# Performance work log

Measured on AMD Instinct MI355X. Metric: run time of the kernel, lower is better.

Reference implementation:

```python
import jax, jax.numpy as jnp
import numpy as np

# Dimensions (match init_kwargs / input_specs)
B, T, H, S, R, E = 4, 2048, 1024, 512, 16, 4
F = 6 + 2 * R           # engine_state_feature_dim
ETA = 0.1               # impression_rate
ACC_DECAY = 0.99        # accumulator EMA decay
EPS = 1e-6


def setup_inputs() -> dict:
    key = jax.random.key(0)
    ks = jax.random.split(key, 20)
    n = jax.random.normal
    x = n(ks[0], (B, T, H), jnp.float32)
    # ComplexLinear signal_proj: hidden -> state
    sig_Wr = n(ks[1], (H, S), jnp.float32) / np.sqrt(H).astype(np.float32)
    sig_Wi = n(ks[2], (H, S), jnp.float32) / np.sqrt(H).astype(np.float32)
    sig_br = jnp.zeros((S,), jnp.float32)
    sig_bi = jnp.zeros((S,), jnp.float32)
    # Per-engine complex state projection [E, S, R] and diagonal complex decay [E, R]
    A_r = n(ks[3], (E, S, R), jnp.float32) / np.sqrt(S).astype(np.float32)
    A_i = n(ks[4], (E, S, R), jnp.float32) / np.sqrt(S).astype(np.float32)
    mag = 0.90 + 0.09 * jax.random.uniform(ks[5], (E, R), jnp.float32)
    ph = (2.0 * np.pi) * jax.random.uniform(ks[6], (E, R), jnp.float32)
    lam_r = mag * jnp.cos(ph)
    lam_i = mag * jnp.sin(ph)
    # Per-engine ComplexLinear: feature(F) -> hidden(H)
    eh_Wr = n(ks[7], (E, F, H), jnp.float32) / np.sqrt(F).astype(np.float32)
    eh_Wi = n(ks[8], (E, F, H), jnp.float32) / np.sqrt(F).astype(np.float32)
    eh_br = jnp.zeros((E, H), jnp.float32)
    eh_bi = jnp.zeros((E, H), jnp.float32)
    # Engine fusion ComplexLinear: E*H -> H
    fu_Wr = n(ks[9], (E * H, H), jnp.float32) / np.sqrt(E * H).astype(np.float32)
    fu_Wi = n(ks[10], (E * H, H), jnp.float32) / np.sqrt(E * H).astype(np.float32)
    fu_br = jnp.zeros((H,), jnp.float32)
    fu_bi = jnp.zeros((H,), jnp.float32)
    # Gate: Linear(4H -> H)
    g_W = n(ks[11], (4 * H, H), jnp.float32) / np.sqrt(4 * H).astype(np.float32)
    g_b = jnp.zeros((H,), jnp.float32)
    return dict(x=x, sig_Wr=sig_Wr, sig_Wi=sig_Wi, sig_br=sig_br, sig_bi=sig_bi,
                A_r=A_r, A_i=A_i, lam_r=lam_r, lam_i=lam_i,
                eh_Wr=eh_Wr, eh_Wi=eh_Wi, eh_br=eh_br, eh_bi=eh_bi,
                fu_Wr=fu_Wr, fu_Wi=fu_Wi, fu_br=fu_br, fu_bi=fu_bi,
                g_W=g_W, g_b=g_b)


def _run_engines(ur, ui, lam_r, lam_i):
    """Complex diagonal recurrence over time for all engines jointly.
    ur, ui: [E,B,T,R] complex drive. Returns per-step features [E,B,T,F] (real, imag)."""
    lr = lam_r[:, None, :]  # [E,1,R]
    li = lam_i[:, None, :]

    def step(carry, u):
        hr, hi, acc = carry                      # [E,B,R], [E,B,R], [E,B]
        ur_t, ui_t = u                           # [E,B,R]
        nhr = (1.0 - ETA) * (lr * hr - li * hi) + ETA * ur_t
        nhi = (1.0 - ETA) * (lr * hi + li * hr) + ETA * ui_t
        mag2 = nhr * nhr + nhi * nhi             # [E,B,R]
        m_mean = jnp.mean(mag2, axis=-1)         # [E,B]
        nacc = ACC_DECAY * acc + (1.0 - ACC_DECAY) * m_mean
        inv = jax.lax.rsqrt(m_mean + EPS)[..., None]
        hnr, hni = nhr * inv, nhi * inv          # rms-normalized complex state
        z = jnp.zeros_like(m_mean)
        scal_r = jnp.stack([hnr.mean(-1), hni.mean(-1),
                            jnp.sqrt(m_mean + EPS),
                            jnp.sqrt(jnp.max(mag2, axis=-1) + EPS),
                            nacc, jnp.log1p(nacc)], axis=-1)   # [E,B,6]
        scal_i = jnp.stack([hni.mean(-1), -hnr.mean(-1), z, z, z, z], axis=-1)
        fr = jnp.concatenate([scal_r, hnr, hni], axis=-1)      # [E,B,F]
        fi = jnp.concatenate([scal_i, hni, -hnr], axis=-1)
        return (nhr, nhi, nacc), (fr, fi)

    init = (jnp.zeros((E, B, R), ur.dtype), jnp.zeros((E, B, R), ur.dtype),
            jnp.zeros((E, B), ur.dtype))
    u_seq = (jnp.moveaxis(ur, 2, 0), jnp.moveaxis(ui, 2, 0))   # [T,E,B,R]
    _, (frs, fis) = jax.lax.scan(step, init, u_seq)
    return jnp.moveaxis(frs, 0, 2), jnp.moveaxis(fis, 0, 2)    # [E,B,T,F]


def reference(x, sig_Wr, sig_Wi, sig_br, sig_bi, A_r, A_i, lam_r, lam_i,
              eh_Wr, eh_Wi, eh_br, eh_bi, fu_Wr, fu_Wi, fu_br, fu_bi, g_W, g_b):
    # Complex signal projection of real input: z = (Wr + i Wi)^T x + b
    zr = x @ sig_Wr + sig_br                     # [B,T,S]
    zi = x @ sig_Wi + sig_bi
    # Complex per-engine drive u = A^H-style complex matmul: [E,B,T,R]
    ur = jnp.einsum('bts,esr->ebtr', zr, A_r) - jnp.einsum('bts,esr->ebtr', zi, A_i)
    ui = jnp.einsum('bts,esr->ebtr', zr, A_i) + jnp.einsum('bts,esr->ebtr', zi, A_r)
    fr, fi = _run_engines(ur, ui, lam_r, lam_i)  # [E,B,T,F]
    # Per-engine ComplexLinear feature -> hidden
    yr = (jnp.einsum('ebtf,efh->ebth', fr, eh_Wr)
          - jnp.einsum('ebtf,efh->ebth', fi, eh_Wi)) + eh_br[:, None, None, :]
    yi = (jnp.einsum('ebtf,efh->ebth', fr, eh_Wi)
          + jnp.einsum('ebtf,efh->ebth', fi, eh_Wr)) + eh_bi[:, None, None, :]
    # Concat engines along feature axis -> [B,T,E*H]
    yr_c = jnp.moveaxis(yr, 0, 2).reshape(B, T, E * H)
    yi_c = jnp.moveaxis(yi, 0, 2).reshape(B, T, E * H)
    # Engine fusion ComplexLinear
    frf = yr_c @ fu_Wr - yi_c @ fu_Wi + fu_br    # [B,T,H]
    fif = yr_c @ fu_Wi + yi_c @ fu_Wr + fu_bi
    mag = jnp.sqrt(frf * frf + fif * fif + EPS)
    g = jax.nn.sigmoid(jnp.concatenate([x, frf, fif, mag], axis=-1) @ g_W + g_b)
    return g * frf + (1.0 - g) * x
```

## Files before the change

### kernel.cpp

```cpp
#include <hip/hip_runtime.h>
#include <stdint.h>

#define B_ 4
#define T_ 2048
#define H_ 1024
#define S_ 512
#define R_ 16
#define E_ 4
#define F_ 38
#define BT_ (B_*T_)
#define KF_ 320

typedef __attribute__((ext_vector_type(8))) __bf16 bf16x8;
typedef __attribute__((ext_vector_type(4))) float f32x4;

static __device__ __forceinline__ unsigned short f2bf(float f) {
    unsigned int u = __float_as_uint(f);
    unsigned int r = (u + 0x7fffu + ((u >> 16) & 1u)) >> 16;
    return (unsigned short)r;
}

static __device__ __forceinline__ void gload_lds16(const unsigned short* g, unsigned short* l) {
    __builtin_amdgcn_global_load_lds(
        (const __attribute__((address_space(1))) unsigned int*)g,
        (__attribute__((address_space(3))) unsigned int*)l, 16, 0, 0);
}

template<int EPI>
__global__ __launch_bounds__(256) void k_gemm(
    const unsigned short* __restrict__ A, int lda,
    const unsigned short* __restrict__ BT, int ldb,
    float* __restrict__ C, int ldc,
    const float* __restrict__ bias, int K,
    size_t sA, size_t sB, size_t sC, int nbx,
    const float* __restrict__ aux1, const float* __restrict__ aux2,
    unsigned short* __restrict__ auxO)
{
    A  += (size_t)blockIdx.z * sA;
    BT += (size_t)blockIdx.z * sB;
    C  += (size_t)blockIdx.z * sC;

    int bx, by;
    {
        const int f = blockIdx.x;
        const int nwg = gridDim.x;
        int s;
        if ((nwg & 7) == 0) {
            const int q = nwg >> 3;
            s = (f & 7) * q + (f >> 3);
        } else s = f;
        by = s / nbx; bx = s - by * nbx;
    }

    __shared__ unsigned short As[128 * 32];
    __shared__ unsigned short Bs[128 * 32];
    const int tid = threadIdx.x;
    const int l = tid & 63;
    const int wv = tid >> 6;
    const int wm = wv >> 1, wn = wv & 1;
    const int m16 = l & 15, kg = l >> 4;
    const size_t bm = (size_t)by * 128;
    const size_t bn = (size_t)bx * 128;

    const int slab0 = wv * 2, slab1 = wv * 2 + 1;
    const int rIn = l >> 2;
    const int kOff = (l & 3) * 8;
    const unsigned short* gA0 = A + (bm + slab0 * 16 + rIn) * (size_t)lda + kOff;
    const unsigned short* gA1 = A + (bm + slab1 * 16 + rIn) * (size_t)lda + kOff;
    const unsigned short* gB0 = BT + (bn + slab0 * 16 + rIn) * (size_t)ldb + kOff;
    const unsigned short* gB1 = BT + (bn + slab1 * 16 + rIn) * (size_t)ldb + kOff;
    unsigned short* lA0 = As + slab0 * 512;
    unsigned short* lA1 = As + slab1 * 512;
    unsigned short* lB0 = Bs + slab0 * 512;
    unsigned short* lB1 = Bs + slab1 * 512;

    f32x4 acc[4][4];
#pragma unroll
    for (int i = 0; i < 4; ++i)
#pragma unroll
        for (int j = 0; j < 4; ++j) acc[i][j] = (f32x4){0.f, 0.f, 0.f, 0.f};

    const int nkt = K >> 5;
    for (int kt = 0; kt < nkt; ++kt) {
        gload_lds16(gA0, lA0);
        gload_lds16(gA1, lA1);
        gload_lds16(gB0, lB0);
        gload_lds16(gB1, lB1);
        gA0 += 32; gA1 += 32; gB0 += 32; gB1 += 32;
        __syncthreads();
        bf16x8 af[4], bfr[4];
#pragma unroll
        for (int i = 0; i < 4; ++i)
            af[i] = *(const bf16x8*)&As[(wm * 64 + i * 16 + m16) * 32 + kg * 8];
#pragma unroll
        for (int j = 0; j < 4; ++j)
            bfr[j] = *(const bf16x8*)&Bs[(wn * 64 + j * 16 + m16) * 32 + kg * 8];
#pragma unroll
        for (int i = 0; i < 4; ++i)
#pragma unroll
            for (int j = 0; j < 4; ++j)
                acc[i][j] = __builtin_amdgcn_mfma_f32_16x16x32_bf16(af[i], bfr[j], acc[i][j], 0, 0, 0);
        __syncthreads();
    }

#pragma unroll
    for (int j = 0; j < 4; ++j) {
        const size_t col = bn + wn * 64 + j * 16 + m16;
        const float bv = (EPI == 1) ? 0.f : (bias ? bias[col] : 0.f);
#pragma unroll
        for (int i = 0; i < 4; ++i) {
            const size_t row0 = bm + wm * 64 + i * 16 + kg * 4;
#pragma unroll
            for (int p = 0; p < 4; ++p) {
                const size_t row = row0 + p;
                if constexpr (EPI == 0) {
                    C[row * (size_t)ldc + col] = acc[i][j][p] + bv;
                } else if constexpr (EPI == 1) {
                    atomicAdd(&C[row * (size_t)ldc + col], acc[i][j][p]);
                } else if constexpr (EPI == 2) {
                    const float v = acc[i][j][p] + bv;
                    const float w = __shfl_xor(v, 1, 64);
                    const int h = (int)(col >> 1);
                    if ((col & 1) == 0) {
                        C[row * 1024 + h] = v;
                        auxO[row * 4096 + 1024 + h] = f2bf(v);
                    } else {
                        auxO[row * 4096 + 2048 + h] = f2bf(v);
                        auxO[row * 4096 + 3072 + h] = f2bf(sqrtf(w * w + v * v + 1e-6f));
                    }
                } else {
                    const float z = acc[i][j][p] + bv;
                    const float g = 1.f / (1.f + __expf(-z));
                    const float fr = aux1[row * 1024 + col];
                    const float xv = aux2[row * 1024 + col];
                    C[row * 1024 + col] = fmaf(g, fr - xv, xv);
                }
            }
        }
    }
}

__global__ __launch_bounds__(256) void k_cast_x(const float* __restrict__ x,
                                                unsigned short* __restrict__ Abig)
{
    const int gid = blockIdx.x * 256 + threadIdx.x;
    const int row = gid >> 8;
    const int c4 = (gid & 255) << 2;
    float4 v = *(const float4*)&x[(size_t)row * H_ + c4];
    ushort4 o;
    o.x = f2bf(v.x); o.y = f2bf(v.y); o.z = f2bf(v.z); o.w = f2bf(v.w);
    *(ushort4*)&Abig[(size_t)row * 4096 + c4] = o;
}

__global__ __launch_bounds__(256) void k_gwt(const float* __restrict__ gW,
                                             unsigned short* __restrict__ gWT)
{
    __shared__ float tile[32][33];
    const int tx = threadIdx.x & 31, ty = threadIdx.x >> 5;
    const int k0 = blockIdx.x * 32, n0 = blockIdx.y * 32;
#pragma unroll
    for (int q = 0; q < 4; ++q) {
        int kk = ty * 4 + q;
        tile[kk][tx] = gW[(size_t)(k0 + kk) * H_ + n0 + tx];
    }
    __syncthreads();
#pragma unroll
    for (int q = 0; q < 4; ++q) {
        int nn = ty * 4 + q;
        gWT[(size_t)(n0 + nn) * 4096 + k0 + tx] = f2bf(tile[tx][nn]);
    }
}

__global__ __launch_bounds__(64) void k_wu(const float* __restrict__ sigWr,
                                           const float* __restrict__ sigWi,
                                           const float* __restrict__ A_r,
                                           const float* __restrict__ A_i,
                                           unsigned short* __restrict__ WuT)
{
    __shared__ float swr[S_], swi[S_];
    const int h = blockIdx.x;
    const int tid = threadIdx.x;
    for (int s = tid; s < S_; s += 64) {
        swr[s] = sigWr[(size_t)h * S_ + s];
        swi[s] = sigWi[(size_t)h * S_ + s];
    }
    __syncthreads();
    const int e = tid >> 4, r = tid & 15;
    float a0 = 0.f, a1 = 0.f;
    for (int s = 0; s < S_; ++s) {
        float ar = A_r[((size_t)(e * S_ + s)) * R_ + r];
        float ai = A_i[((size_t)(e * S_ + s)) * R_ + r];
        float wr = swr[s], wi = swi[s];
        a0 += wr * ar - wi * ai;
        a1 += wr * ai + wi * ar;
    }
    WuT[(size_t)tid * H_ + h] = f2bf(a0);
    WuT[(size_t)(64 + tid) * H_ + h] = f2bf(a1);
}

__global__ __launch_bounds__(64) void k_bu(const float* __restrict__ sigbr,
                                           const float* __restrict__ sigbi,
                                           const float* __restrict__ A_r,
                                           const float* __restrict__ A_i,
                                           float* __restrict__ b_u)
{
    const int n = blockIdx.x;
    const int lane = threadIdx.x;
    const int m = n & 63;
    const int e = m >> 4, r = m & 15;
    const bool hi = n >= 64;
    float acc = 0.f;
    for (int s = lane; s < S_; s += 64) {
        float ar = A_r[((size_t)(e * S_ + s)) * R_ + r];
        float ai = A_i[((size_t)(e * S_ + s)) * R_ + r];
        float br = sigbr[s], bi = sigbi[s];
        acc += hi ? (br * ai + bi * ar) : (br * ar - bi * ai);
    }
#pragma unroll
    for (int st = 32; st; st >>= 1) acc += __shfl_down(acc, st, 64);
    if (lane == 0) b_u[n] = acc;
}

__global__ __launch_bounds__(256) void k_uinit(const float* __restrict__ b_u,
                                               float* __restrict__ U)
{
    const int gid = blockIdx.x * 256 + threadIdx.x;
    U[gid] = b_u[gid & 127];
}

__global__ __launch_bounds__(256) void k_prepA(const float* __restrict__ ehWr,
                                               const float* __restrict__ ehWi,
                                               const float* __restrict__ ehbr,
                                               const float* __restrict__ ehbi,
                                               unsigned short* __restrict__ Ac)
{
    const int gid = blockIdx.x * 256 + threadIdx.x;
    const int e = gid >> 16;
    const int rem = gid & 65535;
    const int row = rem >> 9;
    const int k = (rem & 511) << 2;
    float4 f = {0.f, 0.f, 0.f, 0.f};
    if (row < F_) {
        const float* src = (k < 1024) ? ehWr + ((size_t)(e * F_ + row)) * 1024 + k
                                      : ehWi + ((size_t)(e * F_ + row)) * 1024 + (k - 1024);
        f = *(const float4*)src;
    } else if (row == F_) {
        const float* src = (k < 1024) ? ehbr + (size_t)e * 1024 + k
                                      : ehbi + (size_t)e * 1024 + (k - 1024);
        f = *(const float4*)src;
    }
    ushort4 o;
    o.x = f2bf(f.x); o.y = f2bf(f.y); o.z = f2bf(f.z); o.w = f2bf(f.w);
    *(ushort4*)&Ac[(size_t)gid * 4] = o;
}

__global__ __launch_bounds__(256) void k_prepB(const float* __restrict__ fuWr,
                                               const float* __restrict__ fuWi,
                                               unsigned short* __restrict__ Bc)
{
    __shared__ float tR[32][33], tI[32][33];
    const int e = blockIdx.z;
    const int k0 = blockIdx.x * 32;
    const int h0 = blockIdx.y * 32;
    const int tx = threadIdx.x & 31, ty = threadIdx.x >> 5;
    const float* fr = fuWr + ((size_t)e * 1024 + k0) * 1024 + h0;
    const float* fi = fuWi + ((size_t)e * 1024 + k0) * 1024 + h0;
#pragma unroll
    for (int q = 0; q < 4; ++q) {
        int kk = ty * 4 + q;
        tR[kk][tx] = fr[(size_t)kk * 1024 + tx];
        tI[kk][tx] = fi[(size_t)kk * 1024 + tx];
    }
    __syncthreads();
    unsigned short* Be = Bc + (size_t)e * 2048 * 2048;
#pragma unroll
    for (int q = 0; q < 4; ++q) {
        int rr = ty * 4 + q;
        float vR = tR[tx][rr], vI = tI[tx][rr];
        size_t rowLo = (size_t)(h0 + rr) * 2048;
        size_t rowHi = (size_t)(1024 + h0 + rr) * 2048;
        Be[rowLo + k0 + tx]        = f2bf(vR);
        Be[rowLo + 1024 + k0 + tx] = f2bf(-vI);
        Be[rowHi + k0 + tx]        = f2bf(vI);
        Be[rowHi + 1024 + k0 + tx] = f2bf(vR);
    }
}

__global__ __launch_bounds__(256) void k_w2t(const float* __restrict__ C,
                                             unsigned short* __restrict__ W2T)
{
    const int gid = blockIdx.x * 256 + threadIdx.x;
    const int n = gid / KF_;
    const int k = gid - n * KF_;
    const int h = n >> 1;
    const int s = n & 1;
    float v = 0.f;
    if (k < 304) {
        const int fp = (k < 152) ? k : k - 152;
        const int e = fp / F_;
        const int f = fp - e * F_;
        const float* Ce = C + ((size_t)e * 128 + f) * 2048;
        const float mr = Ce[h], mi = Ce[1024 + h];
        if (s == 0) v = (k < 152) ? mr : -mi;
        else        v = (k < 152) ? mi :  mr;
    }
    W2T[gid] = f2bf(v);
}

__global__ __launch_bounds__(256) void k_b2(const float* __restrict__ fubr,
                                            const float* __restrict__ fubi,
                                            const float* __restrict__ C,
                                            float* __restrict__ b2)
{
    const int n = blockIdx.x * 256 + threadIdx.x;
    const int h = n >> 1;
    const int s = n & 1;
    const int colOld = s * 1024 + h;
    float v = s ? fubi[h] : fubr[h];
#pragma unroll
    for (int e = 0; e < 4; ++e)
        v += C[(size_t)e * 128 * 2048 + (size_t)F_ * 2048 + colOld];
    b2[n] = v;
}

__global__ __launch_bounds__(64) void k_scan(const float* __restrict__ U,
                                             const float* __restrict__ lam_r,
                                             const float* __restrict__ lam_i,
                                             float* __restrict__ Hr, float* __restrict__ Hi)
{
    const int wid = blockIdx.x;
    const int b = wid >> 6, ch = wid & 63;
    const int lane = threadIdx.x;
    const float cr = 0.9f * lam_r[ch];
    const float ci = 0.9f * lam_i[ch];
    const float* Ub = U + (size_t)b * T_ * 128;
    const int t0 = lane * 32;
    float ur[32], ui[32];
#pragma unroll
    for (int j = 0; j < 32; ++j) {
        ur[j] = Ub[(size_t)(t0 + j) * 128 + ch];
        ui[j] = Ub[(size_t)(t0 + j) * 128 + 64 + ch];
    }
    float hr = 0.f, hi = 0.f;
#pragma unroll
    for (int j = 0; j < 32; ++j) {
        float nr = fmaf(cr, hr, fmaf(-ci, hi, 0.1f * ur[j]));
        float ni = fmaf(cr, hi, fmaf(ci, hr, 0.1f * ui[j]));
        hr = nr; hi = ni;
    }
    float dr = cr, di = ci;
#pragma unroll
    for (int q = 0; q < 5; ++q) { float t = dr*dr - di*di; di = 2.f*dr*di; dr = t; }
    float xr = hr, xi = hi;
#pragma unroll
    for (int st = 1; st < 64; st <<= 1) {
        float yr = __shfl_up(xr, (unsigned)st, 64);
        float yi = __shfl_up(xi, (unsigned)st, 64);
        if (lane >= st) {
            float nxr = fmaf(dr, yr, fmaf(-di, yi, xr));
            float nxi = fmaf(dr, yi, fmaf(di, yr, xi));
            xr = nxr; xi = nxi;
        }
        float t = dr*dr - di*di; di = 2.f*dr*di; dr = t;
    }
    float ir = __shfl_up(xr, 1u, 64);
    float ii = __shfl_up(xi, 1u, 64);
    if (lane == 0) { ir = 0.f; ii = 0.f; }
    hr = ir; hi = ii;
    float* HrB = Hr + (size_t)b * T_ * 64;
    float* HiB = Hi + (size_t)b * T_ * 64;
#pragma unroll
    for (int j = 0; j < 32; ++j) {
        float nr = fmaf(cr, hr, fmaf(-ci, hi, 0.1f * ur[j]));
        float ni = fmaf(cr, hi, fmaf(ci, hr, 0.1f * ui[j]));
        HrB[(size_t)(t0 + j) * 64 + ch] = nr;
        HiB[(size_t)(t0 + j) * 64 + ch] = ni;
        hr = nr; hi = ni;
    }
}

__global__ __launch_bounds__(256) void k_feat(const float* __restrict__ Hr,
                                              const float* __restrict__ Hi,
                                              unsigned short* __restrict__ Fcat,
                                              float* __restrict__ Mbuf)
{
    const int gid = blockIdx.x * 256 + threadIdx.x;
    const int e = gid & 3;
    const int bt = gid >> 2;
    const float* hr = Hr + (size_t)bt * 64 + e * 16;
    const float* hi = Hi + (size_t)bt * 64 + e * 16;
    float nr[16], ni[16];
#pragma unroll
    for (int q = 0; q < 4; ++q) {
        float4 vr = ((const float4*)hr)[q];
        float4 vi = ((const float4*)hi)[q];
        nr[q*4+0]=vr.x; nr[q*4+1]=vr.y; nr[q*4+2]=vr.z; nr[q*4+3]=vr.w;
        ni[q*4+0]=vi.x; ni[q*4+1]=vi.y; ni[q*4+2]=vi.z; ni[q*4+3]=vi.w;
    }
    float sum = 0.f, mx = 0.f, sr = 0.f, si = 0.f;
#pragma unroll
    for (int i = 0; i < 16; ++i) {
        float m2 = nr[i] * nr[i] + ni[i] * ni[i];
        sum += m2; mx = fmaxf(mx, m2);
        sr += nr[i]; si += ni[i];
    }
    const float mm = sum * 0.0625f;
    const float inv = rsqrtf(mm + 1e-6f);
    const int b = bt >> 11, t = bt & (T_ - 1);
    Mbuf[(size_t)(e * 4 + b) * T_ + t] = mm;
    unsigned short* Fp = Fcat + (size_t)bt * KF_;
    const int br = e * F_, bi2 = 152 + e * F_;
    const float mhr = sr * 0.0625f * inv;
    const float mhi = si * 0.0625f * inv;
    Fp[br + 0] = f2bf(mhr);
    Fp[br + 1] = f2bf(mhi);
    Fp[br + 2] = f2bf(sqrtf(mm + 1e-6f));
    Fp[br + 3] = f2bf(sqrtf(mx + 1e-6f));
    Fp[bi2 + 0] = f2bf(mhi);
    Fp[bi2 + 1] = f2bf(-mhr);
#pragma unroll
    for (int i = 0; i < 16; ++i) {
        float a = nr[i] * inv, c = ni[i] * inv;
        Fp[br + 6 + i]   = f2bf(a);
        Fp[br + 22 + i]  = f2bf(c);
        Fp[bi2 + 6 + i]  = f2bf(c);
        Fp[bi2 + 22 + i] = f2bf(-a);
    }
}

__global__ __launch_bounds__(256) void k_acc(const float* __restrict__ Mbuf,
                                             unsigned short* __restrict__ Fcat)
{
    const int w = blockIdx.x * 4 + (threadIdx.x >> 6);
    const int lane = threadIdx.x & 63;
    const int e = w >> 2, b = w & 3;
    const float* mp = Mbuf + (size_t)(e * 4 + b) * T_ + lane * 32;
    float m[32];
#pragma unroll
    for (int j = 0; j < 32; ++j) m[j] = mp[j];
    float s = 0.f;
#pragma unroll
    for (int j = 0; j < 32; ++j) s = fmaf(0.99f, s, 0.01f * m[j]);
    float d = 0.99f;
#pragma unroll
    for (int q = 0; q < 5; ++q) d = d * d;
    float x = s;
#pragma unroll
    for (int st = 1; st < 64; st <<= 1) {
        float y = __shfl_up(x, (unsigned)st, 64);
        if (lane >= st) x = fmaf(d, y, x);
        d = d * d;
    }
    float init = __shfl_up(x, 1u, 64);
    if (lane == 0) init = 0.f;
    float acc = init;
#pragma unroll
    for (int j = 0; j < 32; ++j) {
        acc = fmaf(0.99f, acc, 0.01f * m[j]);
        const int t = lane * 32 + j;
        size_t ro = ((size_t)(b * T_ + t)) * KF_ + e * F_;
        Fcat[ro + 4] = f2bf(acc);
        Fcat[ro + 5] = f2bf(log1pf(acc));
    }
}

extern "C" void kernel_launch(void* const* d_in, const int* in_sizes, int n_in,
                              void* d_out, int out_size, void* d_ws, size_t ws_size,
                              hipStream_t stream)
{
    const float* x     = (const float*)d_in[0];
    const float* sigWr = (const float*)d_in[1];
    const float* sigWi = (const float*)d_in[2];
    const float* sigbr = (const float*)d_in[3];
    const float* sigbi = (const float*)d_in[4];
    const float* A_r   = (const float*)d_in[5];
    const float* A_i   = (const float*)d_in[6];
    const float* lam_r = (const float*)d_in[7];
    const float* lam_i = (const float*)d_in[8];
    const float* ehWr  = (const float*)d_in[9];
    const float* ehWi  = (const float*)d_in[10];
    const float* ehbr  = (const float*)d_in[11];
    const float* ehbi  = (const float*)d_in[12];
    const float* fuWr  = (const float*)d_in[13];
    const float* fuWi  = (const float*)d_in[14];
    const float* fubr  = (const float*)d_in[15];
    const float* fubi  = (const float*)d_in[16];
    const float* gW    = (const float*)d_in[17];
    const float* gb    = (const float*)d_in[18];

    char* ws = (char*)d_ws;
    size_t off = 0;
    auto alloc = [&](size_t bytes) -> void* {
        void* p = ws + off;
        off = (off + bytes + 255) & ~(size_t)255;
        return p;
    };
    unsigned short* Abig = (unsigned short*)alloc((size_t)BT_ * 4096 * 2);
    float* FRFr          = (float*)alloc((size_t)BT_ * 1024 * 4);
    unsigned short* Fcat = (unsigned short*)alloc((size_t)BT_ * KF_ * 2);
    float* U             = (float*)alloc((size_t)BT_ * 128 * 4);
    float* Hr            = (float*)alloc((size_t)BT_ * 64 * 4);
    float* Hi            = (float*)alloc((size_t)BT_ * 64 * 4);
    float* Mbuf          = (float*)alloc((size_t)16 * T_ * 4);
    unsigned short* WuT  = (unsigned short*)alloc((size_t)128 * H_ * 2);
    float* b_u           = (float*)alloc(128 * 4);
    unsigned short* W2T  = (unsigned short*)alloc((size_t)2048 * KF_ * 2);
    float* b2            = (float*)alloc(2048 * 4);
    unsigned short* gWT  = (unsigned short*)alloc((size_t)H_ * 4096 * 2);
    unsigned short* Acomp= (unsigned short*)alloc((size_t)4 * 128 * 2048 * 2);
    unsigned short* Bcomp= (unsigned short*)alloc((size_t)4 * 2048 * 2048 * 2);
    float* Ccomp         = (float*)alloc((size_t)4 * 128 * 2048 * 4);
    if (off > ws_size) return;

    hipMemsetAsync(Fcat, 0, (size_t)BT_ * KF_ * 2, stream);

    k_cast_x<<<dim3(BT_ * H_ / 4 / 256), dim3(256), 0, stream>>>(x, Abig);
    k_gwt<<<dim3(128, 32), dim3(256), 0, stream>>>(gW, gWT);
    k_wu<<<dim3(H_), dim3(64), 0, stream>>>(sigWr, sigWi, A_r, A_i, WuT);
    k_bu<<<dim3(128), dim3(64), 0, stream>>>(sigbr, sigbi, A_r, A_i, b_u);
    k_prepA<<<dim3(1024), dim3(256), 0, stream>>>(ehWr, ehWi, ehbr, ehbi, Acomp);
    k_prepB<<<dim3(32, 32, 4), dim3(256), 0, stream>>>(fuWr, fuWi, Bcomp);

    k_gemm<0><<<dim3(16, 1, 4), dim3(256), 0, stream>>>(
        Acomp, 2048, Bcomp, 2048, Ccomp, 2048, (const float*)nullptr, 2048,
        (size_t)128 * 2048, (size_t)2048 * 2048, (size_t)128 * 2048, 16,
        nullptr, nullptr, nullptr);

    k_w2t<<<dim3(2048 * KF_ / 256), dim3(256), 0, stream>>>(Ccomp, W2T);
    k_b2<<<dim3(8), dim3(256), 0, stream>>>(fubr, fubi, Ccomp, b2);

    k_uinit<<<dim3(BT_ * 128 / 256), dim3(256), 0, stream>>>(b_u, U);
    k_gemm<1><<<dim3(64, 1, 4), dim3(256), 0, stream>>>(
        Abig, 4096, WuT, H_, U, 128, (const float*)nullptr, 256,
        (size_t)256, (size_t)256, (size_t)0, 1, nullptr, nullptr, nullptr);

    k_scan<<<dim3(B_ * 64), dim3(64), 0, stream>>>(U, lam_r, lam_i, Hr, Hi);
    k_feat<<<dim3(BT_ * E_ / 256), dim3(256), 0, stream>>>(Hr, Hi, Fcat, Mbuf);
    k_acc<<<dim3(4), dim3(256), 0, stream>>>(Mbuf, Fcat);

    k_gemm<2><<<dim3(1024, 1, 1), dim3(256), 0, stream>>>(
        Fcat, KF_, W2T, KF_, FRFr, 1024, b2, KF_,
        (size_t)0, (size_t)0, (size_t)0, 16, nullptr, nullptr, Abig);

    k_gemm<3><<<dim3(512, 1, 1), dim3(256), 0, stream>>>(
        Abig, 4096, gWT, 4096, (float*)d_out, 1024, gb, 4096,
        (size_t)0, (size_t)0, (size_t)0, 8, FRFr, x, nullptr);
}
```

Before: 412.3 us.

## Switch GEMM to register-prefetched padded LDS tiles with templated K-tile size

```diff
diff --git a/kernel.cpp b/kernel.cpp
--- a/kernel.cpp
+++ b/kernel.cpp
@@ -20,59 +20,42 @@
     return (unsigned short)r;
 }
 
-static __device__ __forceinline__ void gload_lds16(const unsigned short* g, unsigned short* l) {
-    __builtin_amdgcn_global_load_lds(
-        (const __attribute__((address_space(1))) unsigned int*)g,
-        (__attribute__((address_space(3))) unsigned int*)l, 16, 0, 0);
-}
-
-template<int EPI>
+template<int EPI, int BK>
 __global__ __launch_bounds__(256) void k_gemm(
     const unsigned short* __restrict__ A, int lda,
     const unsigned short* __restrict__ BT, int ldb,
     float* __restrict__ C, int ldc,
     const float* __restrict__ bias, int K,
-    size_t sA, size_t sB, size_t sC, int nbx,
+    size_t sA, size_t sB, size_t sC, size_t sA2, size_t sB2, int zShift,
     const float* __restrict__ aux1, const float* __restrict__ aux2,
     unsigned short* __restrict__ auxO)
 {
-    A  += (size_t)blockIdx.z * sA;
-    BT += (size_t)blockIdx.z * sB;
-    C  += (size_t)blockIdx.z * sC;
-
-    int bx, by;
-    {
-        const int f = blockIdx.x;
-        const int nwg = gridDim.x;
-        int s;
-        if ((nwg & 7) == 0) {
-            const int q = nwg >> 3;
-            s = (f & 7) * q + (f >> 3);
-        } else s = f;
-        by = s / nbx; bx = s - by * nbx;
-    }
-
-    __shared__ unsigned short As[128 * 32];
-    __shared__ unsigned short Bs[128 * 32];
+    constexpr int LDP = BK + 8;
+    constexpr int L   = BK / 16;
+    constexpr int TPR = BK / 8;
+    constexpr int RPP = 256 / TPR;
+
+    const int z1 = (int)blockIdx.z >> zShift;
+    const int z0 = (int)blockIdx.z & ((1 << zShift) - 1);
+    A  += (size_t)z1 * sA + (size_t)z0 * sA2;
+    BT += (size_t)z1 * sB + (size_t)z0 * sB2;
+    C  += (size_t)z1 * sC;
+
+    __shared__ unsigned short As[128 * LDP];
+    __shared__ unsigned short Bs[128 * LDP];
     const int tid = threadIdx.x;
     const int l = tid & 63;
     const int wv = tid >> 6;
     const int wm = wv >> 1, wn = wv & 1;
     const int m16 = l & 15, kg = l >> 4;
-    const size_t bm = (size_t)by * 128;
-    const size_t bn = (size_t)bx * 128;
-
-    const int slab0 = wv * 2, slab1 = wv * 2 + 1;
-    const int rIn = l >> 2;
-    const int kOff = (l & 3) * 8;
-    const unsigned short* gA0 = A + (bm + slab0 * 16 + rIn) * (size_t)lda + kOff;
-    const unsigned short* gA1 = A + (bm + slab1 * 16 + rIn) * (size_t)lda + kOff;
-    const unsigned short* gB0 = BT + (bn + slab0 * 16 + rIn) * (size_t)ldb + kOff;
-    const unsigned short* gB1 = BT + (bn + slab1 * 16 + rIn) * (size_t)ldb + kOff;
-    unsigned short* lA0 = As + slab0 * 512;
-    unsigned short* lA1 = As + slab1 * 512;
-    unsigned short* lB0 = Bs + slab0 * 512;
-    unsigned short* lB1 = Bs + slab1 * 512;
+    const size_t bm = (size_t)blockIdx.y * 128;
+    const size_t bn = (size_t)blockIdx.x * 128;
+
+    const int rS = tid / TPR;
+    const int kS = (tid % TPR) * 8;
+    const unsigned short* gA = A + (bm + rS) * (size_t)lda + kS;
+    const unsigned short* gB = BT + (bn + rS) * (size_t)ldb + kS;
+    const int sBase = rS * LDP + kS;
 
     f32x4 acc[4][4];
 #pragma unroll
@@ -80,27 +63,45 @@
 #pragma unroll
         for (int j = 0; j < 4; ++j) acc[i][j] = (f32x4){0.f, 0.f, 0.f, 0.f};
 
-    const int nkt = K >> 5;
+    uint4 rA[L], rB[L];
+#pragma unroll
+    for (int p = 0; p < L; ++p) {
+        rA[p] = *(const uint4*)(gA + (size_t)p * RPP * lda);
+        rB[p] = *(const uint4*)(gB + (size_t)p * RPP * ldb);
+    }
+
+    const int nkt = K / BK;
     for (int kt = 0; kt < nkt; ++kt) {
-        gload_lds16(gA0, lA0);
-        gload_lds16(gA1, lA1);
-        gload_lds16(gB0, lB0);
-        gload_lds16(gB1, lB1);
-        gA0 += 32; gA1 += 32; gB0 += 32; gB1 += 32;
         __syncthreads();
-        bf16x8 af[4], bfr[4];
-#pragma unroll
-        for (int i = 0; i < 4; ++i)
-            af[i] = *(const bf16x8*)&As[(wm * 64 + i * 16 + m16) * 32 + kg * 8];
-#pragma unroll
-        for (int j = 0; j < 4; ++j)
-            bfr[j] = *(const bf16x8*)&Bs[(wn * 64 + j * 16 + m16) * 32 + kg * 8];
-#pragma unroll
-        for (int i = 0; i < 4; ++i)
+#pragma unroll
+        for (int p = 0; p < L; ++p) {
+            *(uint4*)&As[sBase + p * RPP * LDP] = rA[p];
+            *(uint4*)&Bs[sBase + p * RPP * LDP] = rB[p];
+        }
+        if (kt + 1 < nkt) {
+            gA += BK; gB += BK;
+#pragma unroll
+            for (int p = 0; p < L; ++p) {
+                rA[p] = *(const uint4*)(gA + (size_t)p * RPP * lda);
+                rB[p] = *(const uint4*)(gB + (size_t)p * RPP * ldb);
+            }
+        }
+        __syncthreads();
+#pragma unroll
+        for (int ks = 0; ks < BK / 32; ++ks) {
+            bf16x8 af[4], bfr[4];
+#pragma unroll
+            for (int i = 0; i < 4; ++i)
+                af[i] = *(const bf16x8*)&As[(wm * 64 + i * 16 + m16) * LDP + ks * 32 + kg * 8];
 #pragma unroll
             for (int j = 0; j < 4; ++j)
-                acc[i][j] = __builtin_amdgcn_mfma_f32_16x16x32_bf16(af[i], bfr[j], acc[i][j], 0, 0, 0);
-        __syncthreads();
+                bfr[j] = *(const bf16x8*)&Bs[(wn * 64 + j * 16 + m16) * LDP + ks * 32 + kg * 8];
+#pragma unroll
+            for (int i = 0; i < 4; ++i)
+#pragma unroll
+                for (int j = 0; j < 4; ++j)
+                    acc[i][j] = __builtin_amdgcn_mfma_f32_16x16x32_bf16(af[i], bfr[j], acc[i][j], 0, 0, 0);
+        }
     }
 
 #pragma unroll
@@ -521,28 +522,31 @@
     k_prepA<<<dim3(1024), dim3(256), 0, stream>>>(ehWr, ehWi, ehbr, ehbi, Acomp);
     k_prepB<<<dim3(32, 32, 4), dim3(256), 0, stream>>>(fuWr, fuWi, Bcomp);
 
-    k_gemm<0><<<dim3(16, 1, 4), dim3(256), 0, stream>>>(
+    k_gemm<0, 64><<<dim3(16, 1, 4), dim3(256), 0, stream>>>(
         Acomp, 2048, Bcomp, 2048, Ccomp, 2048, (const float*)nullptr, 2048,
-        (size_t)128 * 2048, (size_t)2048 * 2048, (size_t)128 * 2048, 16,
-        nullptr, nullptr, nullptr);
+        (size_t)128 * 2048, (size_t)2048 * 2048, (size_t)128 * 2048,
+        (size_t)0, (size_t)0, 0, nullptr, nullptr, nullptr);
 
     k_w2t<<<dim3(2048 * KF_ / 256), dim3(256), 0, stream>>>(Ccomp, W2T);
     k_b2<<<dim3(8), dim3(256), 0, stream>>>(fubr, fubi, Ccomp, b2);
 
     k_uinit<<<dim3(BT_ * 128 / 256), dim3(256), 0, stream>>>(b_u, U);
-    k_gemm<1><<<dim3(64, 1, 4), dim3(256), 0, stream>>>(
+    k_gemm<1, 32><<<dim3(1, 64, 4), dim3(256), 0, stream>>>(
         Abig, 4096, WuT, H_, U, 128, (const float*)nullptr, 256,
-        (size_t)256, (size_t)256, (size_t)0, 1, nullptr, nullptr, nullptr);
+        (size_t)0, (size_t)0, (size_t)0, (size_t)256, (size_t)256, 2,
+        nullptr, nullptr, nullptr);
 
     k_scan<<<dim3(B_ * 64), dim3(64), 0, stream>>>(U, lam_r, lam_i, Hr, Hi);
     k_feat<<<dim3(BT_ * E_ / 256), dim3(256), 0, stream>>>(Hr, Hi, Fcat, Mbuf);
     k_acc<<<dim3(4), dim3(256), 0, stream>>>(Mbuf, Fcat);
 
-    k_gemm<2><<<dim3(1024, 1, 1), dim3(256), 0, stream>>>(
+    k_gemm<2, 32><<<dim3(16, 64), dim3(256), 0, stream>>>(
         Fcat, KF_, W2T, KF_, FRFr, 1024, b2, KF_,
-        (size_t)0, (size_t)0, (size_t)0, 16, nullptr, nullptr, Abig);
-
-    k_gemm<3><<<dim3(512, 1, 1), dim3(256), 0, stream>>>(
+        (size_t)0, (size_t)0, (size_t)0, (size_t)0, (size_t)0, 0,
+        nullptr, nullptr, Abig);
+
+    k_gemm<3, 64><<<dim3(8, 64), dim3(256), 0, stream>>>(
         Abig, 4096, gWT, 4096, (float*)d_out, 1024, gb, 4096,
-        (size_t)0, (size_t)0, (size_t)0, 8, FRFr, x, nullptr);
-}
+        (size_t)0, (size_t)0, (size_t)0, (size_t)0, (size_t)0, 0,
+        FRFr, x, nullptr);
+}
```

Result: slower. 678.5 us (+64.6%).
